# Optimization experiments

Measured on AMD Instinct MI355X. Metric: run time of the kernel, lower is better.

## Reference

```python
import jax, jax.numpy as jnp
import numpy as np

BATCH = 1024
SEQ = 512
HID = 512
OUT = 10


def setup_inputs() -> dict:
    key = jax.random.key(0)
    k1, k2, k3, k4 = jax.random.split(key, 4)
    # Xavier-ish scaled params (scale irrelevant for correctness baseline)
    x = jax.random.normal(k1, (BATCH, SEQ), dtype=jnp.float32)
    W_hx = jax.random.normal(k2, (HID, 1), dtype=jnp.float32) * (1.0 / np.sqrt(1 + HID)).astype(np.float32)
    W_hh = jax.random.normal(k3, (HID, HID), dtype=jnp.float32) * (1.0 / np.sqrt(2 * HID)).astype(np.float32)
    W_yh = jax.random.normal(k4, (OUT, HID), dtype=jnp.float32) * (1.0 / np.sqrt(HID + OUT)).astype(np.float32)
    b_h = jnp.zeros((HID, 1), dtype=jnp.float32)
    b_y = jnp.zeros((OUT, 1), dtype=jnp.float32)
    return {"x": x, "W_hx": W_hx, "W_hh": W_hh, "W_yh": W_yh, "b_h": b_h, "b_y": b_y}


def reference(x, W_hx, W_hh, W_yh, b_h, b_y):
    # x: [B, T]; hidden state h: [H, B] (column-major layout as in the torch code)
    B = x.shape[0]
    H = W_hh.shape[0]
    xs = x.T  # [T, B], scan over time

    def step(h, x_t):
        # x_t: [B] -> treated as [1, B]; W_hx: [H, 1]
        h_new = jnp.tanh(W_hx @ x_t[None, :] + W_hh @ h + b_h)  # [H, B]
        return h_new, None

    h0 = jnp.zeros((H, B), dtype=x.dtype)
    h_T, _ = jax.lax.scan(step, h0, xs)
    y = W_yh @ h_T + b_y  # [O, B] — only the last timestep's output is returned
    return y.T  # [B, O]
```

## Files before the change

### kernel.cpp

```cpp
#include <hip/hip_runtime.h>


#define BATCH 1024
#define SEQT  512
#define HID   512
#define OUTD  10
#define KR    12
#define NKK   16

typedef _Float16 f16;
typedef _Float16 f16x8 __attribute__((ext_vector_type(8)));
typedef _Float16 f16x4 __attribute__((ext_vector_type(4)));
typedef float    f32x4 __attribute__((ext_vector_type(4)));

__global__ void wconv_kernel(const float* __restrict__ Whh, f16* __restrict__ frag) {
    int id = blockIdx.x * blockDim.x + threadIdx.x;
    int lane = id & 63;
    int kk   = (id >> 6) & 15;
    int mt   = (id >> 10) & 3;
    int g    = id >> 12;
    int m = g * 64 + mt * 16 + (lane & 15);
    int k = kk * 32 + ((lane >> 4) & 3) * 8;
    const float* src = Whh + (size_t)m * HID + k;
    f16x8 v;
#pragma unroll
    for (int j = 0; j < 8; ++j) v[j] = (f16)src[j];
    *(f16x8*)(frag + (size_t)id * 8) = v;
}

__device__ __forceinline__ float fast_tanh(float v) {
    v = fminf(fmaxf(v, -15.f), 15.f);
    float e = __expf(2.f * v);
    return (e - 1.f) * __builtin_amdgcn_rcpf(e + 1.f);
}

__global__ __launch_bounds__(512)
__attribute__((amdgpu_waves_per_eu(2, 2)))
void rnn_cu(
    const f16* __restrict__ frag,
    f16* __restrict__ hG,
    const float* __restrict__ x,
    const float* __restrict__ Whx,
    const float* __restrict__ bh)
{
    __shared__ f16 HB[2][8192];
    __shared__ f16 WL[65536];

    const int tid  = threadIdx.x;
    const int w    = tid >> 6;
    const int lane = tid & 63;
    const int n    = lane & 15;
    const int q    = lane >> 4;
    const int bg   = blockIdx.x;

    {
        f16x8 z;
#pragma unroll
        for (int j = 0; j < 8; ++j) z[j] = (f16)0.f;
        *(f16x8*)&HB[0][tid * 16]     = z;
        *(f16x8*)&HB[0][tid * 16 + 8] = z;
    }

    const f16x8* A = (const f16x8*)frag;

#pragma unroll
    for (int mt = 0; mt < 4; ++mt)
#pragma unroll
        for (int kkl = 0; kkl < 4; ++kkl) {
            int e = ((w * 4 + mt) * 4 + kkl) * 64 + lane;
            *(f16x8*)&WL[e * 8] = A[((w * 4 + mt) * 16 + (KR + kkl)) * 64 + lane];
        }

    f16x8 Wr[KR * 4];
#pragma unroll
    for (int kk = 0; kk < KR; ++kk)
#pragma unroll
        for (int mt = 0; mt < 4; ++mt)
            Wr[kk * 4 + mt] = A[((w * 4 + mt) * 16 + kk) * 64 + lane];

    f16x4 wx_h[4], bh_h[4];
#pragma unroll
    for (int mt = 0; mt < 4; ++mt) {
        int m0 = w * 64 + mt * 16 + q * 4;
        f32x4 w4 = *(const f32x4*)(Whx + m0);
        f32x4 b4 = *(const f32x4*)(bh + m0);
#pragma unroll
        for (int r = 0; r < 4; ++r) {
            wx_h[mt][r] = (f16)w4[r];
            bh_h[mt][r] = (f16)b4[r];
        }
    }

    __syncthreads();

    const int b = bg * 16 + n;
    const float* xp = x + (size_t)b * SEQT;

#pragma unroll 1
    for (int s = 0; s < SEQT; ++s) {
        const f16* hbr = &HB[s & 1][0];
        f16*       hbw = &HB[(s & 1) ^ 1][0];

        float xv = xp[s];

        f32x4 acc[4] = {{0,0,0,0},{0,0,0,0},{0,0,0,0},{0,0,0,0}};

#pragma unroll
        for (int kk = 0; kk < KR; ++kk) {
            f16x8 bf = *(const f16x8*)&hbr[(kk * 64 + lane) * 8];
#pragma unroll
            for (int mt = 0; mt < 4; ++mt)
                acc[mt] = __builtin_amdgcn_mfma_f32_16x16x32_f16(
                    Wr[kk * 4 + mt], bf, acc[mt], 0, 0, 0);
        }
#pragma unroll
        for (int kkl = 0; kkl < 4; ++kkl) {
            f16x8 bf = *(const f16x8*)&hbr[((KR + kkl) * 64 + lane) * 8];
#pragma unroll
            for (int mt = 0; mt < 4; ++mt) {
                f16x8 a = *(const f16x8*)&WL[(((w * 4 + mt) * 4 + kkl) * 64 + lane) * 8];
                acc[mt] = __builtin_amdgcn_mfma_f32_16x16x32_f16(
                    a, bf, acc[mt], 0, 0, 0);
            }
        }

#pragma unroll
        for (int mt = 0; mt < 4; ++mt) {
            f16x4 hv;
#pragma unroll
            for (int r = 0; r < 4; ++r) {
                float pre = fmaf((float)wx_h[mt][r], xv, acc[mt][r])
                          + (float)bh_h[mt][r];
                hv[r] = (f16)fast_tanh(pre);
            }
            int kkd = w * 2 + (mt >> 1);
            int q2  = (mt & 1) * 2 + (q >> 1);
            int j0  = (q & 1) * 4;
            int off = (kkd * 64 + q2 * 16 + n) * 8 + j0;
            if (s < SEQT - 1) {
                *(f16x4*)&hbw[off] = hv;
            } else {
                *(f16x4*)(hG + (size_t)(((bg * 16 + kkd) * 64 + q2 * 16 + n) * 8 + j0)) = hv;
            }
        }

        __syncthreads();
    }
}

__global__ __launch_bounds__(256) void y_kernel(
    const f16* __restrict__ h, const float* __restrict__ Wyh,
    const float* __restrict__ by, float* __restrict__ out)
{
    int id = blockIdx.x * blockDim.x + threadIdx.x;
    if (id >= BATCH * OUTD) return;
    int b = id / OUTD, o = id % OUTD;
    int bg = b >> 4, n = b & 15;
    const float* wrow = Wyh + (size_t)o * HID;
    float s = by[o];
    for (int kk = 0; kk < 16; ++kk)
#pragma unroll
        for (int q2 = 0; q2 < 4; ++q2) {
            f16x8 hv = *(const f16x8*)(h + (size_t)((bg * 16 + kk) * 64 + q2 * 16 + n) * 8);
            const float* wp = wrow + kk * 32 + q2 * 8;
#pragma unroll
            for (int j = 0; j < 8; ++j) s += wp[j] * (float)hv[j];
        }
    out[id] = s;
}

extern "C" void kernel_launch(void* const* d_in, const int* in_sizes, int n_in,
                              void* d_out, int out_size, void* d_ws, size_t ws_size,
                              hipStream_t stream) {
    const float* x   = (const float*)d_in[0];
    const float* Whx = (const float*)d_in[1];
    const float* Whh = (const float*)d_in[2];
    const float* Wyh = (const float*)d_in[3];
    const float* bh  = (const float*)d_in[4];
    const float* by  = (const float*)d_in[5];
    float* out = (float*)d_out;

    char* ws   = (char*)d_ws;
    f16*  hG   = (f16*)ws;
    f16*  frag = (f16*)(ws + (2 << 20));

    wconv_kernel<<<128, 256, 0, stream>>>(Whh, frag);
    rnn_cu<<<64, 512, 0, stream>>>(frag, hG, x, Whx, bh);
    y_kernel<<<(BATCH * OUTD + 255) / 256, 256, 0, stream>>>(hG, Wyh, by, out);
}
```

Measured before the change: 1.333 ms.

## Halve RNN block to 4 waves, each computing 128 rows with deeper register weights

The recurrent kernel now runs 256 threads (4 waves) per block, each wave owning 128 hidden rows (8 MFMA tiles). Six tiles keep their full-K weight fragments in registers and two stream from LDS, with a 3-deep software prefetch ring for the h and LDS weight fragments. Wx and bias are packed as f16 pairs by a new prep kernel and reloaded from global memory each step instead of being held in registers. The aim is to cut the per-step barrier cost across fewer waves and to hide LDS latency, at the cost of heavy register pressure (96 weight vectors per lane) and less wave-level parallelism per CU.

```diff
diff --git a/kernel.cpp b/kernel.cpp
--- a/kernel.cpp
+++ b/kernel.cpp
@@ -5,8 +5,6 @@
 #define SEQT  512
 #define HID   512
 #define OUTD  10
-#define KR    12
-#define NKK   16
 
 typedef _Float16 f16;
 typedef _Float16 f16x8 __attribute__((ext_vector_type(8)));
@@ -17,15 +15,24 @@
     int id = blockIdx.x * blockDim.x + threadIdx.x;
     int lane = id & 63;
     int kk   = (id >> 6) & 15;
-    int mt   = (id >> 10) & 3;
-    int g    = id >> 12;
-    int m = g * 64 + mt * 16 + (lane & 15);
+    int rg   = id >> 10;
+    int m = rg * 16 + (lane & 15);
     int k = kk * 32 + ((lane >> 4) & 3) * 8;
     const float* src = Whh + (size_t)m * HID + k;
     f16x8 v;
 #pragma unroll
     for (int j = 0; j < 8; ++j) v[j] = (f16)src[j];
     *(f16x8*)(frag + (size_t)id * 8) = v;
+}
+
+__global__ void prep_kernel(const float* __restrict__ Whx,
+                            const float* __restrict__ bh,
+                            f16* __restrict__ wxbh) {
+    int m = blockIdx.x * blockDim.x + threadIdx.x;
+    if (m < HID) {
+        wxbh[2 * m]     = (f16)Whx[m];
+        wxbh[2 * m + 1] = (f16)bh[m];
+    }
 }
 
 __device__ __forceinline__ float fast_tanh(float v) {
@@ -34,14 +41,13 @@
     return (e - 1.f) * __builtin_amdgcn_rcpf(e + 1.f);
 }
 
-__global__ __launch_bounds__(512)
-__attribute__((amdgpu_waves_per_eu(2, 2)))
+__global__ __launch_bounds__(256)
+__attribute__((amdgpu_waves_per_eu(1, 1)))
 void rnn_cu(
     const f16* __restrict__ frag,
     f16* __restrict__ hG,
     const float* __restrict__ x,
-    const float* __restrict__ Whx,
-    const float* __restrict__ bh)
+    const f16* __restrict__ wxbh)
 {
     __shared__ f16 HB[2][8192];
     __shared__ f16 WL[65536];
@@ -57,90 +63,96 @@
         f16x8 z;
 #pragma unroll
         for (int j = 0; j < 8; ++j) z[j] = (f16)0.f;
-        *(f16x8*)&HB[0][tid * 16]     = z;
-        *(f16x8*)&HB[0][tid * 16 + 8] = z;
+#pragma unroll
+        for (int i = 0; i < 4; ++i) *(f16x8*)&HB[0][tid * 32 + i * 8] = z;
     }
 
     const f16x8* A = (const f16x8*)frag;
 
 #pragma unroll
-    for (int mt = 0; mt < 4; ++mt)
-#pragma unroll
-        for (int kkl = 0; kkl < 4; ++kkl) {
-            int e = ((w * 4 + mt) * 4 + kkl) * 64 + lane;
-            *(f16x8*)&WL[e * 8] = A[((w * 4 + mt) * 16 + (KR + kkl)) * 64 + lane];
-        }
-
-    f16x8 Wr[KR * 4];
-#pragma unroll
-    for (int kk = 0; kk < KR; ++kk)
-#pragma unroll
-        for (int mt = 0; mt < 4; ++mt)
-            Wr[kk * 4 + mt] = A[((w * 4 + mt) * 16 + kk) * 64 + lane];
-
-    f16x4 wx_h[4], bh_h[4];
-#pragma unroll
-    for (int mt = 0; mt < 4; ++mt) {
-        int m0 = w * 64 + mt * 16 + q * 4;
-        f32x4 w4 = *(const f32x4*)(Whx + m0);
-        f32x4 b4 = *(const f32x4*)(bh + m0);
-#pragma unroll
-        for (int r = 0; r < 4; ++r) {
-            wx_h[mt][r] = (f16)w4[r];
-            bh_h[mt][r] = (f16)b4[r];
-        }
-    }
+    for (int i = 0; i < 32; ++i) {
+        int e    = i * 256 + tid;
+        int slot = e >> 10;
+        int kk   = (e >> 6) & 15;
+        int ln   = e & 63;
+        int rg   = (slot >> 1) * 8 + 6 + (slot & 1);
+        *(f16x8*)&WL[(size_t)e * 8] = A[(rg * 16 + kk) * 64 + ln];
+    }
+
+    f16x8 Wr[96];
+#pragma unroll
+    for (int kk = 0; kk < 16; ++kk)
+#pragma unroll
+        for (int mt = 0; mt < 6; ++mt)
+            Wr[kk * 6 + mt] = A[((w * 8 + mt) * 16 + kk) * 64 + lane];
 
     __syncthreads();
 
-    const int b = bg * 16 + n;
-    const float* xp = x + (size_t)b * SEQT;
+    const float* xp = x + (size_t)(bg * 16 + n) * SEQT;
+    const int a6base = (w * 2) * 1024 + lane;
+    const int a7base = (w * 2 + 1) * 1024 + lane;
 
 #pragma unroll 1
     for (int s = 0; s < SEQT; ++s) {
         const f16* hbr = &HB[s & 1][0];
         f16*       hbw = &HB[(s & 1) ^ 1][0];
-
         float xv = xp[s];
 
-        f32x4 acc[4] = {{0,0,0,0},{0,0,0,0},{0,0,0,0},{0,0,0,0}};
-
-#pragma unroll
-        for (int kk = 0; kk < KR; ++kk) {
-            f16x8 bf = *(const f16x8*)&hbr[(kk * 64 + lane) * 8];
-#pragma unroll
-            for (int mt = 0; mt < 4; ++mt)
+        int wo = 0;
+        asm volatile("" : "+v"(wo));
+
+        f32x4 acc[8];
+#pragma unroll
+        for (int mt = 0; mt < 8; ++mt) acc[mt] = (f32x4){0.f, 0.f, 0.f, 0.f};
+
+        f16x8 bfp[3], a6p[3], a7p[3];
+#pragma unroll
+        for (int i = 0; i < 3; ++i) {
+            bfp[i] = *(const f16x8*)&hbr[(i * 64 + lane) * 8];
+            a6p[i] = *(const f16x8*)&WL[(size_t)(a6base + i * 64 + wo) * 8];
+            a7p[i] = *(const f16x8*)&WL[(size_t)(a7base + i * 64 + wo) * 8];
+        }
+
+#pragma unroll
+        for (int kk = 0; kk < 16; ++kk) {
+            const int c = kk % 3;
+#pragma unroll
+            for (int mt = 0; mt < 6; ++mt)
                 acc[mt] = __builtin_amdgcn_mfma_f32_16x16x32_f16(
-                    Wr[kk * 4 + mt], bf, acc[mt], 0, 0, 0);
-        }
-#pragma unroll
-        for (int kkl = 0; kkl < 4; ++kkl) {
-            f16x8 bf = *(const f16x8*)&hbr[((KR + kkl) * 64 + lane) * 8];
-#pragma unroll
-            for (int mt = 0; mt < 4; ++mt) {
-                f16x8 a = *(const f16x8*)&WL[(((w * 4 + mt) * 4 + kkl) * 64 + lane) * 8];
-                acc[mt] = __builtin_amdgcn_mfma_f32_16x16x32_f16(
-                    a, bf, acc[mt], 0, 0, 0);
+                    Wr[kk * 6 + mt], bfp[c], acc[mt], 0, 0, 0);
+            acc[6] = __builtin_amdgcn_mfma_f32_16x16x32_f16(a6p[c], bfp[c], acc[6], 0, 0, 0);
+            acc[7] = __builtin_amdgcn_mfma_f32_16x16x32_f16(a7p[c], bfp[c], acc[7], 0, 0, 0);
+            if (kk < 13) {
+                bfp[c] = *(const f16x8*)&hbr[((kk + 3) * 64 + lane) * 8];
+                a6p[c] = *(const f16x8*)&WL[(size_t)(a6base + (kk + 3) * 64 + wo) * 8];
+                a7p[c] = *(const f16x8*)&WL[(size_t)(a7base + (kk + 3) * 64 + wo) * 8];
             }
         }
 
-#pragma unroll
-        for (int mt = 0; mt < 4; ++mt) {
+        const f16* wp = wxbh;
+        asm volatile("" : "+v"(wp));
+        f16x8 wb[8];
+#pragma unroll
+        for (int mt = 0; mt < 8; ++mt)
+            wb[mt] = *(const f16x8*)(wp + (size_t)(w * 128 + mt * 16 + q * 4) * 2);
+
+#pragma unroll
+        for (int mt = 0; mt < 8; ++mt) {
             f16x4 hv;
 #pragma unroll
             for (int r = 0; r < 4; ++r) {
-                float pre = fmaf((float)wx_h[mt][r], xv, acc[mt][r])
-                          + (float)bh_h[mt][r];
+                float pre = fmaf((float)wb[mt][2 * r], xv, acc[mt][r])
+                          + (float)wb[mt][2 * r + 1];
                 hv[r] = (f16)fast_tanh(pre);
             }
-            int kkd = w * 2 + (mt >> 1);
-            int q2  = (mt & 1) * 2 + (q >> 1);
+            int kkb = w * 4 + (mt >> 1);
+            int hi  = (mt & 1) * 2 + (q >> 1);
             int j0  = (q & 1) * 4;
-            int off = (kkd * 64 + q2 * 16 + n) * 8 + j0;
+            int off = (kkb * 64 + hi * 16 + n) * 8 + j0;
             if (s < SEQT - 1) {
                 *(f16x4*)&hbw[off] = hv;
             } else {
-                *(f16x4*)(hG + (size_t)(((bg * 16 + kkd) * 64 + q2 * 16 + n) * 8 + j0)) = hv;
+                *(f16x4*)(hG + (size_t)(((bg * 16 + kkb) * 64 + hi * 16 + n) * 8 + j0)) = hv;
             }
         }
 
@@ -182,9 +194,11 @@
 
     char* ws   = (char*)d_ws;
     f16*  hG   = (f16*)ws;
-    f16*  frag = (f16*)(ws + (2 << 20));
+    f16*  frag = (f16*)(ws + (1 << 20));
+    f16*  wxbh = (f16*)(ws + (3 << 19));
 
     wconv_kernel<<<128, 256, 0, stream>>>(Whh, frag);
-    rnn_cu<<<64, 512, 0, stream>>>(frag, hG, x, Whx, bh);
+    prep_kernel<<<2, 256, 0, stream>>>(Whx, bh, wxbh);
+    rnn_cu<<<64, 256, 0, stream>>>(frag, hG, x, wxbh);
     y_kernel<<<(BATCH * OUTD + 255) / 256, 256, 0, stream>>>(hG, Wyh, by, out);
 }
```

New measurement: 1.628 ms. 1.22x slower.

## Replace per-step block barrier with per-wave flag dataflow sync

Applied to the files above, without the earlier changes.

Removes the __syncthreads at the end of each timestep. Each wave now publishes a step counter in global flags after writing its two hidden-state k-slices. Consumer waves spin on those flags just before reading each slice, and each wave rotates its k-order to start with its own slices. Whx/bias are pre-packed to f16 in a separate kernel and re-read per step instead of kept in registers, freeing registers. This adds polling cost, relies on relaxed atomics plus LDS write visibility across waves, and includes a spin-budget escape.

```diff
diff --git a/kernel.cpp b/kernel.cpp
--- a/kernel.cpp
+++ b/kernel.cpp
@@ -5,8 +5,6 @@
 #define SEQT  512
 #define HID   512
 #define OUTD  10
-#define KR    12
-#define NKK   16
 
 typedef _Float16 f16;
 typedef _Float16 f16x8 __attribute__((ext_vector_type(8)));
@@ -28,6 +26,16 @@
     *(f16x8*)(frag + (size_t)id * 8) = v;
 }
 
+__global__ void prep_kernel(const float* __restrict__ Whx,
+                            const float* __restrict__ bh,
+                            f16* __restrict__ wxbh) {
+    int m = blockIdx.x * blockDim.x + threadIdx.x;
+    if (m < HID) {
+        wxbh[2 * m]     = (f16)Whx[m];
+        wxbh[2 * m + 1] = (f16)bh[m];
+    }
+}
+
 __device__ __forceinline__ float fast_tanh(float v) {
     v = fminf(fmaxf(v, -15.f), 15.f);
     float e = __expf(2.f * v);
@@ -40,8 +48,8 @@
     const f16* __restrict__ frag,
     f16* __restrict__ hG,
     const float* __restrict__ x,
-    const float* __restrict__ Whx,
-    const float* __restrict__ bh)
+    const f16* __restrict__ wxbh,
+    int* __restrict__ flagsG)
 {
     __shared__ f16 HB[2][8192];
     __shared__ f16 WL[65536];
@@ -52,6 +60,8 @@
     const int n    = lane & 15;
     const int q    = lane >> 4;
     const int bg   = blockIdx.x;
+    const int w2   = w * 2;
+    int* flags = flagsG + bg * 16;
 
     {
         f16x8 z;
@@ -66,74 +76,89 @@
 #pragma unroll
     for (int mt = 0; mt < 4; ++mt)
 #pragma unroll
-        for (int kkl = 0; kkl < 4; ++kkl) {
-            int e = ((w * 4 + mt) * 4 + kkl) * 64 + lane;
-            *(f16x8*)&WL[e * 8] = A[((w * 4 + mt) * 16 + (KR + kkl)) * 64 + lane];
-        }
-
-    f16x8 Wr[KR * 4];
-#pragma unroll
-    for (int kk = 0; kk < KR; ++kk)
+        for (int j = 0; j < 4; ++j) {
+            int kkt = (w2 + 4 * j + 3) & 15;
+            *(f16x8*)&WL[(((w * 4 + mt) * 4 + j) * 64 + lane) * 8] =
+                A[((w * 4 + mt) * 16 + kkt) * 64 + lane];
+        }
+
+    f16x8 Wr[48];
+#pragma unroll
+    for (int t = 0; t < 16; ++t) {
+        if ((t & 3) == 3) continue;
+        int r = t - (t >> 2);
 #pragma unroll
         for (int mt = 0; mt < 4; ++mt)
-            Wr[kk * 4 + mt] = A[((w * 4 + mt) * 16 + kk) * 64 + lane];
-
-    f16x4 wx_h[4], bh_h[4];
-#pragma unroll
-    for (int mt = 0; mt < 4; ++mt) {
-        int m0 = w * 64 + mt * 16 + q * 4;
-        f32x4 w4 = *(const f32x4*)(Whx + m0);
-        f32x4 b4 = *(const f32x4*)(bh + m0);
-#pragma unroll
-        for (int r = 0; r < 4; ++r) {
-            wx_h[mt][r] = (f16)w4[r];
-            bh_h[mt][r] = (f16)b4[r];
-        }
+            Wr[r * 4 + mt] = A[((w * 4 + mt) * 16 + ((w2 + t) & 15)) * 64 + lane];
     }
 
     __syncthreads();
 
-    const int b = bg * 16 + n;
-    const float* xp = x + (size_t)b * SEQT;
+    const float* xp = x + (size_t)(bg * 16 + n) * SEQT;
+    int budget = 1 << 22;
+    int dead = 0;
 
 #pragma unroll 1
     for (int s = 0; s < SEQT; ++s) {
         const f16* hbr = &HB[s & 1][0];
         f16*       hbw = &HB[(s & 1) ^ 1][0];
-
         float xv = xp[s];
 
+        const f16* wlb = &WL[0];
+        asm volatile("" : "+v"(wlb));
+
+        int fl[16];
+        fl[2] = __hip_atomic_load(&flags[(w2 + 2) & 15], __ATOMIC_RELAXED, __HIP_MEMORY_SCOPE_WORKGROUP);
+        fl[3] = __hip_atomic_load(&flags[(w2 + 3) & 15], __ATOMIC_RELAXED, __HIP_MEMORY_SCOPE_WORKGROUP);
+        fl[4] = __hip_atomic_load(&flags[(w2 + 4) & 15], __ATOMIC_RELAXED, __HIP_MEMORY_SCOPE_WORKGROUP);
+        fl[5] = __hip_atomic_load(&flags[(w2 + 5) & 15], __ATOMIC_RELAXED, __HIP_MEMORY_SCOPE_WORKGROUP);
+
         f32x4 acc[4] = {{0,0,0,0},{0,0,0,0},{0,0,0,0},{0,0,0,0}};
 
 #pragma unroll
-        for (int kk = 0; kk < KR; ++kk) {
-            f16x8 bf = *(const f16x8*)&hbr[(kk * 64 + lane) * 8];
-#pragma unroll
-            for (int mt = 0; mt < 4; ++mt)
-                acc[mt] = __builtin_amdgcn_mfma_f32_16x16x32_f16(
-                    Wr[kk * 4 + mt], bf, acc[mt], 0, 0, 0);
-        }
-#pragma unroll
-        for (int kkl = 0; kkl < 4; ++kkl) {
-            f16x8 bf = *(const f16x8*)&hbr[((KR + kkl) * 64 + lane) * 8];
-#pragma unroll
-            for (int mt = 0; mt < 4; ++mt) {
-                f16x8 a = *(const f16x8*)&WL[(((w * 4 + mt) * 4 + kkl) * 64 + lane) * 8];
-                acc[mt] = __builtin_amdgcn_mfma_f32_16x16x32_f16(
-                    a, bf, acc[mt], 0, 0, 0);
-            }
-        }
-
+        for (int t = 0; t < 16; ++t) {
+            const int kkt = (w2 + t) & 15;
+            int zdep = 0;
+            if (t >= 2) {
+                int v = fl[t];
+                while (!dead && v < s) {
+                    v = __hip_atomic_load(&flags[kkt], __ATOMIC_RELAXED, __HIP_MEMORY_SCOPE_WORKGROUP);
+                    if (--budget <= 0) dead = 1;
+                    __builtin_amdgcn_s_sleep(1);
+                }
+                asm("v_and_b32 %0, 0, %1" : "=v"(zdep) : "v"(v));
+            }
+            f16x8 bf = *(const f16x8*)&hbr[(kkt * 64 + lane) * 8 + zdep];
+            if ((t & 3) == 3) {
+                const int j = t >> 2;
+#pragma unroll
+                for (int mt = 0; mt < 4; ++mt) {
+                    f16x8 a = *(const f16x8*)&wlb[(((w * 4 + mt) * 4 + j) * 64 + lane) * 8];
+                    acc[mt] = __builtin_amdgcn_mfma_f32_16x16x32_f16(a, bf, acc[mt], 0, 0, 0);
+                }
+            } else {
+                const int r = t - (t >> 2);
+#pragma unroll
+                for (int mt = 0; mt < 4; ++mt)
+                    acc[mt] = __builtin_amdgcn_mfma_f32_16x16x32_f16(
+                        Wr[r * 4 + mt], bf, acc[mt], 0, 0, 0);
+            }
+            if (t + 4 < 16)
+                fl[t + 4] = __hip_atomic_load(&flags[(w2 + t + 4) & 15], __ATOMIC_RELAXED, __HIP_MEMORY_SCOPE_WORKGROUP);
+        }
+
+        const f16* wp = wxbh;
+        asm volatile("" : "+v"(wp));
 #pragma unroll
         for (int mt = 0; mt < 4; ++mt) {
+            f16x8 wb = *(const f16x8*)(wp + (size_t)(w * 64 + mt * 16 + q * 4) * 2);
             f16x4 hv;
 #pragma unroll
             for (int r = 0; r < 4; ++r) {
-                float pre = fmaf((float)wx_h[mt][r], xv, acc[mt][r])
-                          + (float)bh_h[mt][r];
+                float pre = fmaf((float)wb[2 * r], xv, acc[mt][r]) + (float)wb[2 * r + 1];
                 hv[r] = (f16)fast_tanh(pre);
             }
-            int kkd = w * 2 + (mt >> 1);
+            int kkd = w2 + (mt >> 1);
             int q2  = (mt & 1) * 2 + (q >> 1);
             int j0  = (q & 1) * 4;
             int off = (kkd * 64 + q2 * 16 + n) * 8 + j0;
@@ -144,7 +169,13 @@
             }
         }
 
-        __syncthreads();
+        if (s < SEQT - 1) {
+            asm volatile("s_waitcnt lgkmcnt(0)" ::: "memory");
+            if (lane == 0) {
+                __hip_atomic_store(&flags[w2],     s + 1, __ATOMIC_RELAXED, __HIP_MEMORY_SCOPE_WORKGROUP);
+                __hip_atomic_store(&flags[w2 + 1], s + 1, __ATOMIC_RELAXED, __HIP_MEMORY_SCOPE_WORKGROUP);
+            }
+        }
     }
 }
 
@@ -180,11 +211,15 @@
     const float* by  = (const float*)d_in[5];
     float* out = (float*)d_out;
 
-    char* ws   = (char*)d_ws;
-    f16*  hG   = (f16*)ws;
-    f16*  frag = (f16*)(ws + (2 << 20));
-
+    char* ws    = (char*)d_ws;
+    f16*  hG    = (f16*)ws;
+    f16*  frag  = (f16*)(ws + (1 << 20));
+    f16*  wxbh  = (f16*)(ws + (3 << 19));
+    int*  flags = (int*)(ws + (3 << 19) + (1 << 16));
+
+    hipMemsetAsync(flags, 0, 64 * 16 * sizeof(int), stream);
     wconv_kernel<<<128, 256, 0, stream>>>(Whh, frag);
-    rnn_cu<<<64, 512, 0, stream>>>(frag, hG, x, Whx, bh);
+    prep_kernel<<<2, 256, 0, stream>>>(Whx, bh, wxbh);
+    rnn_cu<<<64, 512, 0, stream>>>(frag, hG, x, wxbh, flags);
     y_kernel<<<(BATCH * OUTD + 255) / 256, 256, 0, stream>>>(hG, Wyh, by, out);
 }
```

Measured after the change: 2.521 ms. +89.2%, slower.
